# Optimization experiments

Measured on AMD Instinct MI355X. Metric: run time of the kernel, lower is better.

The kernel has to match this reference:

```python
import jax, jax.numpy as jnp
import numpy as np

B, C, T, DIN, DOUT = 8, 8, 256, 1536, 512
RADIUS = int(round(0.05 * T))  # radius = round(0.05 * Nframe)
NEG_INF = float(jnp.finfo(jnp.float32).min)


def _suppress_1d(scores):
    # Greedy temporal NMS along T for a single cine. scores: [T]
    order = jnp.argsort(-scores)  # descending
    pos = jnp.arange(T)

    def step(carry, i):
        mask, s = carry
        keep = mask[i]
        window = (jnp.abs(pos - i) <= RADIUS) & (pos != i)
        mask = jnp.where(keep, mask & ~window, mask)
        s = jnp.where(keep, s, s.at[i].set(NEG_INF))
        return (mask, s), None

    (_, s), _ = jax.lax.scan(step, (jnp.ones(T, dtype=bool), scores), order)
    return s


def _top_p_mask(scores, p):
    # scores: [B, Tflat] non-negative; returns float {0,1} mask (detached).
    s = jax.lax.stop_gradient(scores)
    s = jnp.maximum(jnp.where(jnp.isfinite(s), s, 0.0), 0.0)
    sorted_idx = jnp.argsort(-s, axis=-1)
    sorted_s = jnp.take_along_axis(s, sorted_idx, axis=-1)
    norm = sorted_s / (sorted_s.sum(axis=-1, keepdims=True) + 1e-8)
    cum = jnp.cumsum(norm, axis=-1)
    keep = cum <= p
    keep = keep.at[..., :3].set(True)  # always keep top-3
    b_idx = jnp.arange(s.shape[0])[:, None]
    mask = jnp.zeros_like(s, dtype=bool).at[b_idx, sorted_idx].set(keep)
    return mask.astype(scores.dtype)


def setup_inputs() -> dict:
    key = jax.random.key(0)
    ks = jax.random.split(key, 6)
    return {
        "query": jax.random.normal(ks[0], (B, C, T, DIN), dtype=jnp.float32),
        "values": jax.random.normal(ks[1], (B, C, T, DIN), dtype=jnp.float32),
        "W1_w": jax.random.normal(ks[2], (DIN, DOUT), dtype=jnp.float32) / np.sqrt(DIN),
        "W1_b": jax.random.normal(ks[3], (DOUT,), dtype=jnp.float32) * 0.01,
        "V_w": jax.random.normal(ks[4], (DOUT, 1), dtype=jnp.float32) / np.sqrt(DOUT),
        "V_b": jax.random.normal(ks[5], (1,), dtype=jnp.float32) * 0.01,
    }


def reference(query, values, W1_w, W1_b, V_w, V_b):
    # raw_before_suppression = V(tanh(W1(query)))  -> [B, C, T, 1]
    h = jnp.tanh(jnp.einsum('bctd,de->bcte', query, W1_w) + W1_b)
    raw_before = jnp.einsum('bcte,eo->bcto', h, V_w) + V_b

    # greedy temporal suppression, vmapped over B*C cines
    flat = raw_before[..., 0].reshape(B * C, T)
    raw = jax.vmap(_suppress_1d)(flat).reshape(B, C, T, 1)

    score = jax.nn.sigmoid(raw)
    Tflat = C * T
    flat_probs = score[..., 0].reshape(B, Tflat)
    flat_probs = jnp.where(jnp.isfinite(flat_probs), flat_probs, 0.0)

    # eval path: top_p = 0.7 nucleus mask (detached)
    mask = _top_p_mask(flat_probs, 0.7)
    mask = (mask > 0).astype(flat_probs.dtype)

    masked_score = (flat_probs * mask).reshape(B, C, T, 1)
    sum_score = jnp.sum(masked_score, axis=(1, 2), keepdims=True)
    attn = masked_score / (sum_score + 1e-8)
    attn = jnp.where(sum_score <= 0, jnp.full_like(attn, 1.0 / Tflat), attn)

    context = jnp.sum(attn * values, axis=(1, 2))  # [B, DIN]
    return context, attn, masked_score
```

## Files before the change

### kernel.cpp

```cpp
#include <hip/hip_runtime.h>
#include <math.h>
#include <stdint.h>

#define TM 16384
#define NN 512
#define KDIM 1536
#define BM 128
#define BN 128
#define BKS 32
#define NKT 48

typedef _Float16 f16x8 __attribute__((ext_vector_type(8)));
typedef __fp16 h16x2 __attribute__((ext_vector_type(2)));
typedef float f32x4 __attribute__((ext_vector_type(4)));

__device__ __forceinline__ unsigned short f16bits(_Float16 h) {
  union { _Float16 h; unsigned short u; } cv; cv.h = h; return cv.u;
}

__device__ __forceinline__ int swz_chunk(int row, int chunk) {
  return chunk ^ ((row >> 1) & 3);
}

__device__ __forceinline__ void gload_lds16(const void* g, void* l) {
  __builtin_amdgcn_global_load_lds(
      (const __attribute__((address_space(1))) unsigned int*)g,
      (__attribute__((address_space(3))) unsigned int*)l, 16, 0, 0);
}

__global__ __launch_bounds__(256) void convert_w1_kernel(
    const float* __restrict__ W1,
    unsigned short* __restrict__ W1ws)
{
  const int kt = blockIdx.x;
  const int nb = blockIdx.y;
  const int tid = threadIdx.x;
  const int k0 = kt * BKS, n0 = nb * BN;
  const size_t tbase = ((size_t)(nb * NKT + kt) * 2) * 4096;
#pragma unroll
  for (int i = 0; i < 16; ++i) {
    int idx = tid + i * 256;
    int nn = idx & 127, kk = idx >> 7;
    float f = W1[(size_t)(k0 + kk) * NN + n0 + nn];
    _Float16 h = (_Float16)f;
    _Float16 l = (_Float16)((f - (float)h) * 2048.0f);
    int off16 = nn * 32 + (swz_chunk(nn, kk >> 3) << 3) + (kk & 7);
    W1ws[tbase + off16] = f16bits(h);
    W1ws[tbase + 4096 + off16] = f16bits(l);
  }
}

__global__ __launch_bounds__(512, 4) void gemm_score_kernel(
    const float* __restrict__ query,
    const unsigned short* __restrict__ W1ws,
    const float* __restrict__ W1b,
    const float* __restrict__ Vw,
    float* __restrict__ raw_part)
{
  __shared__ __align__(16) char ldsb[2][32768];

  const int tid = threadIdx.x;
  const int lane = tid & 63;
  const int w = tid >> 6;
  const int lrow = lane & 15;
  const int lseg = lane >> 4;

  const int bid = blockIdx.x;
  const int lin = (bid & 7) * 64 + (bid >> 3);
  const int mb = lin >> 2, nb = lin & 3;
  const int m0 = mb * BM, n0 = nb * BN;

  f32x4 zero = {0.f, 0.f, 0.f, 0.f};
  f32x4 acc[8], acc2[8];
#pragma unroll
  for (int n = 0; n < 8; ++n) { acc[n] = zero; acc2[n] = zero; }

  const char* wbase = (const char*)W1ws;

  auto STAGE = [&](int kt, int bufi) {
    char* base = &ldsb[bufi][0];
    const int k0 = kt * BKS;
#pragma unroll
    for (int j = 0; j < 2; ++j) {
      int chunk = (w * 2 + j) * 64 + lane;
      int row = chunk >> 3, cp = chunk & 7;
      int kc = cp ^ (row & 7);
      gload_lds16(query + (size_t)(m0 + row) * KDIM + k0 + kc * 4,
                  base + (w * 2 + j) * 1024);
    }
    const char* tb = wbase + ((size_t)(nb * NKT + kt) * 2) * 8192;
    gload_lds16(tb + w * 1024 + lane * 16, base + 16384 + w * 1024);
    gload_lds16(tb + 8192 + w * 1024 + lane * 16, base + 24576 + w * 1024);
  };

  STAGE(0, 0);
  for (int kt = 0; kt < NKT; ++kt) {
    const int cur = kt & 1;
    if (kt + 1 < NKT) {
      STAGE(kt + 1, cur ^ 1);
      asm volatile("s_waitcnt vmcnt(4)" ::: "memory");
    } else {
      asm volatile("s_waitcnt vmcnt(0)" ::: "memory");
    }
    __builtin_amdgcn_s_barrier();

    const char* base = &ldsb[cur][0];
    f16x8 afh, afl;
    {
      int row = w * 16 + lrow;
      int c0 = (lseg * 2) ^ (row & 7);
      int c1 = (lseg * 2 + 1) ^ (row & 7);
      f32x4 va = *reinterpret_cast<const f32x4*>(base + row * 128 + c0 * 16);
      f32x4 vb = *reinterpret_cast<const f32x4*>(base + row * 128 + c1 * 16);
      union H8 { f16x8 v; h16x2 p[4]; } h, l;
      h.p[0] = __builtin_amdgcn_cvt_pkrtz(va[0], va[1]);
      h.p[1] = __builtin_amdgcn_cvt_pkrtz(va[2], va[3]);
      h.p[2] = __builtin_amdgcn_cvt_pkrtz(vb[0], vb[1]);
      h.p[3] = __builtin_amdgcn_cvt_pkrtz(vb[2], vb[3]);
      float r0 = (va[0] - (float)h.p[0][0]) * 2048.0f;
      float r1 = (va[1] - (float)h.p[0][1]) * 2048.0f;
      float r2 = (va[2] - (float)h.p[1][0]) * 2048.0f;
      float r3 = (va[3] - (float)h.p[1][1]) * 2048.0f;
      float r4 = (vb[0] - (float)h.p[2][0]) * 2048.0f;
      float r5 = (vb[1] - (float)h.p[2][1]) * 2048.0f;
      float r6 = (vb[2] - (float)h.p[3][0]) * 2048.0f;
      float r7 = (vb[3] - (float)h.p[3][1]) * 2048.0f;
      l.p[0] = __builtin_amdgcn_cvt_pkrtz(r0, r1);
      l.p[1] = __builtin_amdgcn_cvt_pkrtz(r2, r3);
      l.p[2] = __builtin_amdgcn_cvt_pkrtz(r4, r5);
      l.p[3] = __builtin_amdgcn_cvt_pkrtz(r6, r7);
      afh = h.v;
      afl = l.v;
    }
#pragma unroll
    for (int nf = 0; nf < 8; ++nf) {
      int brow = nf * 16 + lrow;
      int boff = brow * 64 + (swz_chunk(brow, lseg) << 4);
      f16x8 bh = *reinterpret_cast<const f16x8*>(base + 16384 + boff);
      f16x8 bl = *reinterpret_cast<const f16x8*>(base + 24576 + boff);
      acc[nf]  = __builtin_amdgcn_mfma_f32_16x16x32_f16(afh, bh, acc[nf], 0, 0, 0);
      acc2[nf] = __builtin_amdgcn_mfma_f32_16x16x32_f16(afh, bl, acc2[nf], 0, 0, 0);
      acc2[nf] = __builtin_amdgcn_mfma_f32_16x16x32_f16(afl, bh, acc2[nf], 0, 0, 0);
    }
    asm volatile("s_waitcnt lgkmcnt(0)" ::: "memory");
    __builtin_amdgcn_s_barrier();
  }

  float part[4] = {0.f, 0.f, 0.f, 0.f};
#pragma unroll
  for (int nf = 0; nf < 8; ++nf) {
    int col = n0 + nf * 16 + lrow;
    float bias = W1b[col];
    float vw = Vw[col];
#pragma unroll
    for (int r = 0; r < 4; ++r) {
      float z = acc[nf][r] + acc2[nf][r] * 4.8828125e-4f + bias;
      part[r] += tanhf(z) * vw;
    }
  }
#pragma unroll
  for (int off = 1; off < 16; off <<= 1)
#pragma unroll
    for (int r = 0; r < 4; ++r)
      part[r] += __shfl_xor(part[r], off, 64);
  if (lrow == 0) {
    int rowb = m0 + w * 16 + lseg * 4;
#pragma unroll
    for (int r = 0; r < 4; ++r)
      raw_part[(size_t)nb * TM + rowb + r] = part[r];
  }
}

__global__ __launch_bounds__(64) void nms_kernel(
    const float* __restrict__ raw_part,
    const float* __restrict__ Vb,
    float* __restrict__ probs)
{
  const int cine = blockIdx.x;
  const int lane = threadIdx.x;
  __shared__ float s[256];
  __shared__ int order[256];
  float sv[4];
  const float vb = Vb[0];
#pragma unroll
  for (int q = 0; q < 4; ++q) {
    int p = q * 64 + lane;
    int idx = cine * 256 + p;
    float r = vb;
#pragma unroll
    for (int sl = 0; sl < 4; ++sl) r += raw_part[sl * TM + idx];
    sv[q] = r;
    s[p] = r;
  }
  __syncthreads();
#pragma unroll
  for (int q = 0; q < 4; ++q) {
    int p = q * 64 + lane;
    float st = sv[q];
    int rk = 0;
    for (int j = 0; j < 256; ++j) {
      float sj = s[j];
      rk += (sj > st) || (sj == st && j < p);
    }
    order[rk] = p;
  }
  __syncthreads();
  unsigned m = 0xFu;
  for (int r = 0; r < 256; ++r) {
    int i = order[r];
    int qi = i >> 6, li = i & 63;
    unsigned long long ball = __ballot((lane == li) && ((m >> qi) & 1u));
    if (ball) {
#pragma unroll
      for (int q = 0; q < 4; ++q) {
        int d = q * 64 + lane - i;
        if (d != 0 && d <= 13 && d >= -13) m &= ~(1u << q);
      }
    } else if (lane == li) {
      s[i] = -3.402823466385289e+38f;
    }
  }
  __syncthreads();
#pragma unroll
  for (int q = 0; q < 4; ++q) {
    int p = q * 64 + lane;
    probs[cine * 256 + p] = 1.0f / (1.0f + expf(-s[p]));
  }
}

__global__ __launch_bounds__(256) void topp_kernel(
    const float* __restrict__ probs,
    float* __restrict__ out)
{
  const int b = blockIdx.x;
  const int tid = threadIdx.x;
  __shared__ float p[2048];
  __shared__ int cnz[2048];
  __shared__ float sv[2048];
  __shared__ int sidx[2048];
  __shared__ unsigned char msk[2048];
  __shared__ float red[256];
  __shared__ int nnz_s;

  if (tid == 0) nnz_s = 0;
  for (int i = tid; i < 2048; i += 256) {
    p[i] = probs[b * 2048 + i];
    msk[i] = 0;
  }
  __syncthreads();
  float lsum = 0.f;
  for (int i = tid; i < 2048; i += 256) {
    float v = p[i];
    lsum += v;
    if (v > 0.f) {
      int slot = atomicAdd(&nnz_s, 1);
      cnz[slot] = i;
    }
  }
  red[tid] = lsum;
  __syncthreads();
  for (int sred = 128; sred > 0; sred >>= 1) {
    if (tid < sred) red[tid] += red[tid + sred];
    __syncthreads();
  }
  const int nnz = nnz_s;
  const float total = red[0];
  for (int c = tid; c < nnz; c += 256) {
    int i = cnz[c];
    float pi = p[i];
    int rank = 0;
    for (int cc = 0; cc < nnz; ++cc) {
      int j = cnz[cc];
      float pj = p[j];
      rank += (pj > pi) || (pj == pi && j < i);
    }
    sv[rank] = pi;
    sidx[rank] = i;
  }
  __syncthreads();
  if (tid == 0) {
    float denom = total + 1e-8f;
    float cum = 0.f;
    for (int r = 0; r < nnz; ++r) {
      cum += sv[r] / denom;
      if ((cum <= 0.7f) || (r < 3)) msk[sidx[r]] = 1;
    }
  }
  __syncthreads();
  float ls = 0.f;
  for (int i = tid; i < 2048; i += 256) {
    float m = msk[i] ? p[i] : 0.f;
    sv[i] = m;
    ls += m;
  }
  red[tid] = ls;
  __syncthreads();
  for (int sred = 128; sred > 0; sred >>= 1) {
    if (tid < sred) red[tid] += red[tid + sred];
    __syncthreads();
  }
  const float ssum = red[0];
  const float denom = ssum + 1e-8f;
  const bool uni = (ssum <= 0.f);
  for (int i = tid; i < 2048; i += 256) {
    float m = sv[i];
    out[28672 + b * 2048 + i] = m;
    out[12288 + b * 2048 + i] = uni ? (1.0f / 2048.0f) : (m / denom);
  }
}

__global__ __launch_bounds__(256) void ctx_part_kernel(
    const float* __restrict__ attn,
    const float* __restrict__ values,
    float* __restrict__ ctxp)
{
  const int ch = blockIdx.x % 6;
  const int g  = (blockIdx.x / 6) & 7;
  const int b  = blockIdx.x / 48;
  const int tid = threadIdx.x;
  const int lane = tid & 63, w = tid >> 6;
  __shared__ float av[256];
  __shared__ int   idx[256];
  __shared__ int   wcnt[4];

  float a = attn[b * 2048 + g * 256 + tid];
  unsigned long long mask = __ballot(a != 0.f);
  if (lane == 0) wcnt[w] = __popcll(mask);
  __syncthreads();
  int base = 0;
  for (int i = 0; i < w; ++i) base += wcnt[i];
  if (a != 0.f) {
    int pos = base + __popcll(mask & ((1ull << lane) - 1ull));
    av[pos] = a;
    idx[pos] = g * 256 + tid;
  }
  __syncthreads();
  const int total = wcnt[0] + wcnt[1] + wcnt[2] + wcnt[3];
  const int d = ch * 256 + tid;
  float acc = 0.f;
#pragma unroll 4
  for (int t = 0; t < total; ++t)
    acc += av[t] * values[((size_t)b * 2048 + idx[t]) * KDIM + d];
  ctxp[((size_t)(b * 8 + g)) * KDIM + d] = acc;
}

__global__ __launch_bounds__(256) void ctx_reduce_kernel(
    const float* __restrict__ ctxp,
    float* __restrict__ out)
{
  const int i = blockIdx.x * 256 + threadIdx.x;
  const int b = i / KDIM, d = i % KDIM;
  float sum = 0.f;
#pragma unroll
  for (int g = 0; g < 8; ++g) sum += ctxp[((size_t)(b * 8 + g)) * KDIM + d];
  out[i] = sum;
}

extern "C" void kernel_launch(void* const* d_in, const int* in_sizes, int n_in,
                              void* d_out, int out_size, void* d_ws, size_t ws_size,
                              hipStream_t stream) {
  const float* query  = (const float*)d_in[0];
  const float* values = (const float*)d_in[1];
  const float* W1w    = (const float*)d_in[2];
  const float* W1b    = (const float*)d_in[3];
  const float* Vw     = (const float*)d_in[4];
  const float* Vb     = (const float*)d_in[5];
  float* out = (float*)d_out;

  unsigned short* W1ws = (unsigned short*)d_ws;
  float* raw_part = (float*)((char*)d_ws + 3145728);
  float* probs    = raw_part + 4 * TM;
  float* ctxp     = probs + TM;

  convert_w1_kernel<<<dim3(NKT, 4), 256, 0, stream>>>(W1w, W1ws);
  gemm_score_kernel<<<512, 512, 0, stream>>>(query, W1ws, W1b, Vw, raw_part);
  nms_kernel<<<64, 64, 0, stream>>>(raw_part, Vb, probs);
  topp_kernel<<<8, 256, 0, stream>>>(probs, out);
  ctx_part_kernel<<<384, 256, 0, stream>>>(out + 12288, values, ctxp);
  ctx_reduce_kernel<<<48, 256, 0, stream>>>(ctxp, out);
}
```

Baseline: 166.8 us.

## Load query A-tiles directly to registers and double K-step per barrier

```diff
diff --git a/kernel.cpp b/kernel.cpp
--- a/kernel.cpp
+++ b/kernel.cpp
@@ -9,6 +9,8 @@
 #define BN 128
 #define BKS 32
 #define NKT 48
+#define BK2 64
+#define NKT2 24
 
 typedef _Float16 f16x8 __attribute__((ext_vector_type(8)));
 typedef __fp16 h16x2 __attribute__((ext_vector_type(2)));
@@ -26,6 +28,29 @@
   __builtin_amdgcn_global_load_lds(
       (const __attribute__((address_space(1))) unsigned int*)g,
       (__attribute__((address_space(3))) unsigned int*)l, 16, 0, 0);
+}
+
+__device__ __forceinline__ void conv8(const f32x4 va, const f32x4 vb,
+                                      f16x8& hh, f16x8& ll) {
+  union H8 { f16x8 v; h16x2 p[4]; } h, l;
+  h.p[0] = __builtin_amdgcn_cvt_pkrtz(va[0], va[1]);
+  h.p[1] = __builtin_amdgcn_cvt_pkrtz(va[2], va[3]);
+  h.p[2] = __builtin_amdgcn_cvt_pkrtz(vb[0], vb[1]);
+  h.p[3] = __builtin_amdgcn_cvt_pkrtz(vb[2], vb[3]);
+  float r0 = (va[0] - (float)h.p[0][0]) * 2048.0f;
+  float r1 = (va[1] - (float)h.p[0][1]) * 2048.0f;
+  float r2 = (va[2] - (float)h.p[1][0]) * 2048.0f;
+  float r3 = (va[3] - (float)h.p[1][1]) * 2048.0f;
+  float r4 = (vb[0] - (float)h.p[2][0]) * 2048.0f;
+  float r5 = (vb[1] - (float)h.p[2][1]) * 2048.0f;
+  float r6 = (vb[2] - (float)h.p[3][0]) * 2048.0f;
+  float r7 = (vb[3] - (float)h.p[3][1]) * 2048.0f;
+  l.p[0] = __builtin_amdgcn_cvt_pkrtz(r0, r1);
+  l.p[1] = __builtin_amdgcn_cvt_pkrtz(r2, r3);
+  l.p[2] = __builtin_amdgcn_cvt_pkrtz(r4, r5);
+  l.p[3] = __builtin_amdgcn_cvt_pkrtz(r6, r7);
+  hh = h.v;
+  ll = l.v;
 }
 
 __global__ __launch_bounds__(256) void convert_w1_kernel(
@@ -75,75 +100,79 @@
 #pragma unroll
   for (int n = 0; n < 8; ++n) { acc[n] = zero; acc2[n] = zero; }
 
-  const char* wbase = (const char*)W1ws;
-
-  auto STAGE = [&](int kt, int bufi) {
-    char* base = &ldsb[bufi][0];
-    const int k0 = kt * BKS;
-#pragma unroll
-    for (int j = 0; j < 2; ++j) {
-      int chunk = (w * 2 + j) * 64 + lane;
-      int row = chunk >> 3, cp = chunk & 7;
-      int kc = cp ^ (row & 7);
-      gload_lds16(query + (size_t)(m0 + row) * KDIM + k0 + kc * 4,
-                  base + (w * 2 + j) * 1024);
-    }
-    const char* tb = wbase + ((size_t)(nb * NKT + kt) * 2) * 8192;
-    gload_lds16(tb + w * 1024 + lane * 16, base + 16384 + w * 1024);
-    gload_lds16(tb + 8192 + w * 1024 + lane * 16, base + 24576 + w * 1024);
-  };
-
-  STAGE(0, 0);
-  for (int kt = 0; kt < NKT; ++kt) {
-    const int cur = kt & 1;
-    if (kt + 1 < NKT) {
-      STAGE(kt + 1, cur ^ 1);
-      asm volatile("s_waitcnt vmcnt(4)" ::: "memory");
+  char* const ldsbase = &ldsb[0][0];
+
+  const char* aG = (const char*)(query
+      + (size_t)(m0 + w * 16 + lrow) * KDIM + lseg * 8);
+  const char* bG = (const char*)W1ws + (size_t)(nb * NKT) * 16384
+                   + w * 1024 + lane * 16;
+  const int ldsB = w * 1024;
+  const int x = (lrow >> 1) & 3;
+  const int bro = lrow * 64 + ((lseg ^ x) << 4);
+
+  f32x4 aA0, aA1, aA2, aA3;
+  f32x4 aB0, aB1, aB2, aB3;
+
+  {
+    gload_lds16(bG,         ldsbase + ldsB);
+    gload_lds16(bG + 16384, ldsbase + 8192 + ldsB);
+    gload_lds16(bG + 8192,  ldsbase + 16384 + ldsB);
+    gload_lds16(bG + 24576, ldsbase + 24576 + ldsB);
+    bG += 32768;
+    aA0 = *reinterpret_cast<const f32x4*>(aG);
+    aA1 = *reinterpret_cast<const f32x4*>(aG + 16);
+    aA2 = *reinterpret_cast<const f32x4*>(aG + 128);
+    aA3 = *reinterpret_cast<const f32x4*>(aG + 144);
+    aG += 256;
+  }
+
+  auto STEP = [&](int kt, int cur,
+                  f32x4& c0, f32x4& c1, f32x4& c2, f32x4& c3,
+                  f32x4& n0r, f32x4& n1r, f32x4& n2r, f32x4& n3r) {
+    if (kt + 1 < NKT2) {
+      char* sb = ldsbase + ((cur ^ 1) << 15);
+      gload_lds16(bG,         sb + ldsB);
+      gload_lds16(bG + 16384, sb + 8192 + ldsB);
+      gload_lds16(bG + 8192,  sb + 16384 + ldsB);
+      gload_lds16(bG + 24576, sb + 24576 + ldsB);
+      bG += 32768;
+      n0r = *reinterpret_cast<const f32x4*>(aG);
+      n1r = *reinterpret_cast<const f32x4*>(aG + 16);
+      n2r = *reinterpret_cast<const f32x4*>(aG + 128);
+      n3r = *reinterpret_cast<const f32x4*>(aG + 144);
+      aG += 256;
+      asm volatile("s_waitcnt vmcnt(8)" ::: "memory");
     } else {
       asm volatile("s_waitcnt vmcnt(0)" ::: "memory");
     }
     __builtin_amdgcn_s_barrier();
 
-    const char* base = &ldsb[cur][0];
-    f16x8 afh, afl;
-    {
-      int row = w * 16 + lrow;
-      int c0 = (lseg * 2) ^ (row & 7);
-      int c1 = (lseg * 2 + 1) ^ (row & 7);
-      f32x4 va = *reinterpret_cast<const f32x4*>(base + row * 128 + c0 * 16);
-      f32x4 vb = *reinterpret_cast<const f32x4*>(base + row * 128 + c1 * 16);
-      union H8 { f16x8 v; h16x2 p[4]; } h, l;
-      h.p[0] = __builtin_amdgcn_cvt_pkrtz(va[0], va[1]);
-      h.p[1] = __builtin_amdgcn_cvt_pkrtz(va[2], va[3]);
-      h.p[2] = __builtin_amdgcn_cvt_pkrtz(vb[0], vb[1]);
-      h.p[3] = __builtin_amdgcn_cvt_pkrtz(vb[2], vb[3]);
-      float r0 = (va[0] - (float)h.p[0][0]) * 2048.0f;
-      float r1 = (va[1] - (float)h.p[0][1]) * 2048.0f;
-      float r2 = (va[2] - (float)h.p[1][0]) * 2048.0f;
-      float r3 = (va[3] - (float)h.p[1][1]) * 2048.0f;
-      float r4 = (vb[0] - (float)h.p[2][0]) * 2048.0f;
-      float r5 = (vb[1] - (float)h.p[2][1]) * 2048.0f;
-      float r6 = (vb[2] - (float)h.p[3][0]) * 2048.0f;
-      float r7 = (vb[3] - (float)h.p[3][1]) * 2048.0f;
-      l.p[0] = __builtin_amdgcn_cvt_pkrtz(r0, r1);
-      l.p[1] = __builtin_amdgcn_cvt_pkrtz(r2, r3);
-      l.p[2] = __builtin_amdgcn_cvt_pkrtz(r4, r5);
-      l.p[3] = __builtin_amdgcn_cvt_pkrtz(r6, r7);
-      afh = h.v;
-      afl = l.v;
-    }
-#pragma unroll
-    for (int nf = 0; nf < 8; ++nf) {
-      int brow = nf * 16 + lrow;
-      int boff = brow * 64 + (swz_chunk(brow, lseg) << 4);
-      f16x8 bh = *reinterpret_cast<const f16x8*>(base + 16384 + boff);
-      f16x8 bl = *reinterpret_cast<const f16x8*>(base + 24576 + boff);
-      acc[nf]  = __builtin_amdgcn_mfma_f32_16x16x32_f16(afh, bh, acc[nf], 0, 0, 0);
-      acc2[nf] = __builtin_amdgcn_mfma_f32_16x16x32_f16(afh, bl, acc2[nf], 0, 0, 0);
-      acc2[nf] = __builtin_amdgcn_mfma_f32_16x16x32_f16(afl, bh, acc2[nf], 0, 0, 0);
-    }
+    const char* base = ldsbase + (cur << 15);
+    f16x8 afh[2], afl[2];
+    conv8(c0, c1, afh[0], afl[0]);
+    conv8(c2, c3, afh[1], afl[1]);
+    __builtin_amdgcn_s_setprio(1);
+#pragma unroll
+    for (int s = 0; s < 2; ++s) {
+#pragma unroll
+      for (int nf = 0; nf < 8; ++nf) {
+        const char* p = base + bro + nf * 1024 + s * 8192;
+        f16x8 bh = *reinterpret_cast<const f16x8*>(p);
+        f16x8 bl = *reinterpret_cast<const f16x8*>(p + 16384);
+        acc[nf]  = __builtin_amdgcn_mfma_f32_16x16x32_f16(afh[s], bh, acc[nf], 0, 0, 0);
+        acc2[nf] = __builtin_amdgcn_mfma_f32_16x16x32_f16(afh[s], bl, acc2[nf], 0, 0, 0);
+        acc2[nf] = __builtin_amdgcn_mfma_f32_16x16x32_f16(afl[s], bh, acc2[nf], 0, 0, 0);
+      }
+    }
+    __builtin_amdgcn_s_setprio(0);
     asm volatile("s_waitcnt lgkmcnt(0)" ::: "memory");
     __builtin_amdgcn_s_barrier();
+  };
+
+#pragma unroll 1
+  for (int k2 = 0; k2 < NKT2 / 2; ++k2) {
+    STEP(2 * k2,     0, aA0, aA1, aA2, aA3, aB0, aB1, aB2, aB3);
+    STEP(2 * k2 + 1, 1, aB0, aB1, aB2, aB3, aA0, aA1, aA2, aA3);
   }
 
   float part[4] = {0.f, 0.f, 0.f, 0.f};
```

Measured after the change: 217.4 us. 30.4% more time.
